# Optimization experiments

Measured on AMD Instinct MI355X. Metric: run time of the kernel, lower is better.

The kernel has to match this reference:

```python
import jax, jax.numpy as jnp
import numpy as np

N_EMBD = 1024
EXPAND = 2
D_INNER = N_EMBD * EXPAND          # 2048
D_STATE = 64
N_HEADS = D_INNER // D_STATE       # 32
HEAD_DIM = D_INNER // N_HEADS      # 64
N_GROUPS = 1
D_CONV = 4
N_LAYERS = 48
BATCH, SEQ = 1, 512
PROJ_SIZE = 2 * D_INNER + N_HEADS + 2 * N_GROUPS * D_STATE  # 4256
EPS = 1e-6


def setup_inputs() -> dict:
    key = jax.random.key(0)
    ks = jax.random.split(key, 6)
    init_std = 0.02
    proj_std = 0.02 / np.sqrt(2 * N_LAYERS)
    return {
        "x": jax.random.normal(ks[0], (BATCH, SEQ, N_EMBD), jnp.float32),
        "norm_scale": jnp.ones((N_EMBD,), jnp.float32),
        "w_in": jax.random.normal(ks[1], (N_EMBD, PROJ_SIZE), jnp.float32) * init_std,
        "conv_weight": jax.random.normal(ks[2], (D_CONV, D_INNER), jnp.float32) * 0.02,
        "conv_bias": jnp.zeros((D_INNER,), jnp.float32),
        "A_log": jnp.log(0.5 + jnp.arange(N_HEADS, dtype=jnp.float32) * 0.5 / N_HEADS),
        "dt_bias": jax.random.normal(ks[3], (N_HEADS,), jnp.float32) * 0.1,
        "w_out": jax.random.normal(ks[4], (D_INNER, N_EMBD), jnp.float32) * proj_std,
    }


def _mamba_fwd(x, norm_scale, w_in, conv_weight, conv_bias, A_log, dt_bias, w_out):
    b, T, _ = x.shape
    residual = x
    # RMSNorm
    xn = x * jax.lax.rsqrt(jnp.mean(x * x, axis=-1, keepdims=True) + EPS) * norm_scale
    # in_proj and split
    proj = xn @ w_in  # (b, T, proj_size)
    gate = proj[..., :D_INNER]
    ssm_in = proj[..., D_INNER:2 * D_INNER]
    dt_raw = proj[..., 2 * D_INNER:2 * D_INNER + N_HEADS]
    gs = N_GROUPS * D_STATE
    B = proj[..., 2 * D_INNER + N_HEADS:2 * D_INNER + N_HEADS + gs].reshape(b, T, N_GROUPS, D_STATE)
    C = proj[..., 2 * D_INNER + N_HEADS + gs:].reshape(b, T, N_GROUPS, D_STATE)
    # causal depthwise short conv (cross-correlation, matching lax.conv semantics)
    xp = jnp.pad(ssm_in, ((0, 0), (D_CONV - 1, 0), (0, 0)))
    conv = conv_bias + sum(conv_weight[k] * xp[:, k:k + T, :] for k in range(D_CONV))
    h = jax.nn.silu(conv)  # (b, T, d_inner)
    dt = jax.nn.softplus(dt_raw + dt_bias)  # (b, T, H)
    A = -jnp.exp(A_log)  # (H,)
    A_bar = jnp.exp(A[None, None, :] * dt)  # (b, T, H)
    # heads / groups
    hpg = N_HEADS // N_GROUPS
    xh = h.reshape(b, T, N_HEADS, HEAD_DIM)
    Bh = jnp.repeat(B, hpg, axis=2)  # (b, T, H, N)
    Ch = jnp.repeat(C, hpg, axis=2)  # (b, T, H, N)
    # Bu[b,t,h,p,n] = B[b,t,h,n] * dt[b,t,h] * x[b,t,h,p]
    Bu = Bh[:, :, :, None, :] * (dt[..., None, None] * xh[..., None])  # (b,T,H,P,N)

    def _binary_op(left, right):
        a_l, b_l = left
        a_r, b_r = right
        return (a_l * a_r, a_r * b_l + b_r)

    # A_bar broadcast to (b,T,H,1,1) so the pair broadcasts against Bu
    _, states = jax.lax.associative_scan(_binary_op, (A_bar[..., None, None], Bu), axis=1)
    y = jnp.einsum('bthpn,bthn->bthp', states, Ch).reshape(b, T, D_INNER)
    y = y * jax.nn.silu(gate)
    y = y @ w_out
    return residual + y


def reference(x, norm_scale, w_in, conv_weight, conv_bias, A_log, dt_bias, w_out):
    return _mamba_fwd(x, norm_scale, w_in, conv_weight, conv_bias, A_log, dt_bias, w_out)
```

## Files before the change

### kernel.cpp

```cpp
#include <hip/hip_runtime.h>
#include <hip/hip_bf16.h>

typedef unsigned short u16;
typedef float f32x4v __attribute__((ext_vector_type(4)));
typedef short short8 __attribute__((ext_vector_type(8)));

#define TSEQ 512
#define EMB  1024
#define DI   2048
#define NH   32
#define DS   64
#define PROJ 4256
#define PROJP 4352
#define NCH  16
#define LCH  32
#define KSPLIT2 4

__device__ __forceinline__ u16 f2bf(float f) {
    union { __hip_bfloat16 h; u16 u; } cv;
    cv.h = __float2bfloat16(f);
    return cv.u;
}
__device__ __forceinline__ unsigned pack2(float a, float b) {
    return (unsigned)f2bf(a) | ((unsigned)f2bf(b) << 16);
}
__device__ __forceinline__ float silu(float v) { return v / (1.f + expf(-v)); }

__device__ __forceinline__ void transpose_tile(
        const float* __restrict__ src, u16* __restrict__ dst,
        int K, int N, int n0, int k0, int tid, float tile[64][68]) {
    const int lr = tid >> 4;
    const int lc = tid & 15;
    #pragma unroll
    for (int ps = 0; ps < 4; ++ps) {
        int r = ps * 16 + lr;
        float4 v;
        if (n0 + lc * 4 + 3 < N) {
            v = *(const float4*)&src[(size_t)(k0 + r) * N + n0 + lc * 4];
        } else {
            float t0 = 0.f, t1 = 0.f, t2 = 0.f, t3 = 0.f;
            int nb = n0 + lc * 4;
            if (nb + 0 < N) t0 = src[(size_t)(k0 + r) * N + nb + 0];
            if (nb + 1 < N) t1 = src[(size_t)(k0 + r) * N + nb + 1];
            if (nb + 2 < N) t2 = src[(size_t)(k0 + r) * N + nb + 2];
            if (nb + 3 < N) t3 = src[(size_t)(k0 + r) * N + nb + 3];
            v = make_float4(t0, t1, t2, t3);
        }
        *(float4*)&tile[r][lc * 4] = v;
    }
    __syncthreads();
    const int kk2 = (tid & 31) * 2;
    const int nr  = tid >> 5;
    #pragma unroll
    for (int ps = 0; ps < 8; ++ps) {
        int n = ps * 8 + nr;
        unsigned o = (unsigned)f2bf(tile[kk2][n]) | ((unsigned)f2bf(tile[kk2 + 1][n]) << 16);
        *(unsigned*)&dst[(size_t)(n0 + n) * K + k0 + kk2] = o;
    }
}

__global__ __launch_bounds__(256) void k_prep(
        const float* __restrict__ w_in, u16* __restrict__ w_inT,
        const float* __restrict__ w_out, u16* __restrict__ w_outT,
        const float* __restrict__ x, const float* __restrict__ scale,
        u16* __restrict__ xnb) {
    __shared__ float tile[64][68];
    const int b = blockIdx.x;
    const int tid = threadIdx.x;
    if (b < 1088) {
        int bx = b % 68, by = b / 68;
        transpose_tile(w_in, w_inT, 1024, PROJ, bx * 64, by * 64, tid, tile);
    } else if (b < 1600) {
        int b2 = b - 1088;
        int bx = b2 % 16, by = b2 / 16;
        transpose_tile(w_out, w_outT, 2048, 1024, bx * 64, by * 64, tid, tile);
    } else {
        int t = b - 1600;
        const float4* xr = (const float4*)(x + (size_t)t * EMB);
        float4 v = xr[tid];
        float ss = v.x * v.x + v.y * v.y + v.z * v.z + v.w * v.w;
        #pragma unroll
        for (int off = 32; off; off >>= 1) ss += __shfl_xor(ss, off);
        if ((tid & 63) == 0) tile[0][tid >> 6] = ss;
        __syncthreads();
        float tot = tile[0][0] + tile[0][1] + tile[0][2] + tile[0][3];
        float inv = rsqrtf(tot * (1.f / EMB) + 1e-6f);
        float4 s = ((const float4*)scale)[tid];
        uint2 o;
        o.x = pack2(v.x * inv * s.x, v.y * inv * s.y);
        o.y = pack2(v.z * inv * s.z, v.w * inv * s.w);
        ((uint2*)xnb)[(size_t)t * 256 + tid] = o;
    }
}

template<int BM, int BN>
__global__ __launch_bounds__(256) void k_gemm(
        const u16* __restrict__ A, int lda,
        const u16* __restrict__ BT, int ldb,
        float* __restrict__ C, int ldc, int Kper) {
    constexpr int WM = BM / 2, WN = BN / 2, FM = WM / 16, FN = WN / 16;
    constexpr int NA = BM * 8 / 256, NB = BN * 8 / 256;
    __shared__ __align__(16) u16 Al[BM][72];
    __shared__ __align__(16) u16 Bl[BN][72];
    const int tid = threadIdx.x;
    const int wid = tid >> 6, lane = tid & 63;
    const int wr = wid >> 1, wc = wid & 1;
    const int ar = lane & 15, kg = lane >> 4;
    const int row0 = blockIdx.y * BM, col0 = blockIdx.x * BN;
    const int kbase = blockIdx.z * Kper;
    const int Mtot = gridDim.y * BM;
    float* Cz = C + (size_t)blockIdx.z * Mtot * ldc;

    short8 ra[NA], rb[NB];
    auto load_stage = [&](int k0) {
        #pragma unroll
        for (int j = 0; j < NA; ++j) {
            int idx = tid + j * 256;
            ra[j] = *(const short8*)(A + (size_t)(row0 + (idx >> 3)) * lda + k0 + (idx & 7) * 8);
        }
        #pragma unroll
        for (int j = 0; j < NB; ++j) {
            int idx = tid + j * 256;
            rb[j] = *(const short8*)(BT + (size_t)(col0 + (idx >> 3)) * ldb + k0 + (idx & 7) * 8);
        }
    };
    auto write_stage = [&]() {
        #pragma unroll
        for (int j = 0; j < NA; ++j) {
            int idx = tid + j * 256;
            *(short8*)&Al[idx >> 3][(idx & 7) * 8] = ra[j];
        }
        #pragma unroll
        for (int j = 0; j < NB; ++j) {
            int idx = tid + j * 256;
            *(short8*)&Bl[idx >> 3][(idx & 7) * 8] = rb[j];
        }
    };

    f32x4v acc[FM][FN] = {};
    const int NT = Kper / 64;
    load_stage(kbase);
    for (int kt = 0; kt < NT; ++kt) {
        write_stage();
        __syncthreads();
        if (kt + 1 < NT) load_stage(kbase + (kt + 1) * 64);
        #pragma unroll
        for (int kk = 0; kk < 2; ++kk) {
            short8 af[FM], bf[FN];
            #pragma unroll
            for (int m = 0; m < FM; ++m)
                af[m] = *(const short8*)&Al[wr * WM + m * 16 + ar][kk * 32 + kg * 8];
            #pragma unroll
            for (int n = 0; n < FN; ++n)
                bf[n] = *(const short8*)&Bl[wc * WN + n * 16 + ar][kk * 32 + kg * 8];
            #pragma unroll
            for (int m = 0; m < FM; ++m)
                #pragma unroll
                for (int n = 0; n < FN; ++n)
                    acc[m][n] = __builtin_amdgcn_mfma_f32_16x16x32_bf16(
                        af[m], bf[n], acc[m][n], 0, 0, 0);
        }
        __syncthreads();
    }
    #pragma unroll
    for (int m = 0; m < FM; ++m)
        #pragma unroll
        for (int n = 0; n < FN; ++n)
            #pragma unroll
            for (int j = 0; j < 4; ++j) {
                int row = row0 + wr * WM + m * 16 + kg * 4 + j;
                int col = col0 + wc * WN + n * 16 + ar;
                Cz[(size_t)row * ldc + col] = acc[m][n][j];
            }
}

__global__ __launch_bounds__(256) void k_reduce_out(
        const float* __restrict__ part, const float* __restrict__ x,
        float* __restrict__ out) {
    int i = blockIdx.x * 256 + threadIdx.x;
    float4 v = ((const float4*)x)[i];
    #pragma unroll
    for (int z = 0; z < KSPLIT2; ++z) {
        float4 p = ((const float4*)part)[(size_t)z * (TSEQ * EMB / 4) + i];
        v.x += p.x; v.y += p.y; v.z += p.z; v.w += p.w;
    }
    ((float4*)out)[i] = v;
}

__global__ __launch_bounds__(1024) void k_scan1g(
        const float* __restrict__ proj, const float* __restrict__ cw,
        const float* __restrict__ cb, const float* __restrict__ A_log,
        const float* __restrict__ dt_bias,
        float* __restrict__ Sloc, float* __restrict__ Pcum,
        float* __restrict__ yloc) {
    const int c = blockIdx.x, h = blockIdx.y;
    const int tid = threadIdx.x;
    const int q = tid & 15, p = tid >> 4, n0 = q * 4;
    __shared__ __align__(16) float Blds[LCH][64];
    __shared__ __align__(16) float Clds[LCH][64];
    __shared__ __align__(16) float dtxl[LCH][64];
    __shared__ __align__(16) float xt[LCH + 3][64];
    __shared__ float al[LCH], dl[LCH];
    __shared__ float yl[LCH][64];
    for (int i = tid; i < (LCH + 3) * 64; i += 1024) {
        int r = i >> 6, n = i & 63;
        int tt = c * LCH - 3 + r;
        xt[r][n] = (tt >= 0) ? proj[(size_t)tt * PROJP + DI + h * 64 + n] : 0.f;
    }
    for (int i = tid; i < LCH * 64; i += 1024) {
        int t = i >> 6, n = i & 63;
        Blds[t][n] = proj[(size_t)(c * LCH + t) * PROJP + 2 * DI + NH + n];
        Clds[t][n] = proj[(size_t)(c * LCH + t) * PROJP + 2 * DI + NH + DS + n];
    }
    if (tid < LCH) {
        float z = proj[(size_t)(c * LCH + tid) * PROJP + 2 * DI + h] + dt_bias[h];
        float dt = (z > 20.f) ? z : log1pf(expf(z));
        dl[tid] = dt;
        al[tid] = expf(-expf(A_log[h]) * dt);
    }
    __syncthreads();
    for (int i = tid; i < LCH * 64; i += 1024) {
        int t = i >> 6, pp = i & 63;
        int ch = h * 64 + pp;
        float cv = cb[ch]
                 + cw[0 * DI + ch] * xt[t][pp]     + cw[1 * DI + ch] * xt[t + 1][pp]
                 + cw[2 * DI + ch] * xt[t + 2][pp] + cw[3 * DI + ch] * xt[t + 3][pp];
        dtxl[t][pp] = dl[t] * silu(cv);
    }
    if (tid < LCH) {
        float pr = 1.f;
        #pragma unroll
        for (int k = 0; k < LCH; ++k) if (k <= tid) pr *= al[k];
        Pcum[((size_t)(c * 32 + h)) * LCH + tid] = pr;
    }
    __syncthreads();
    float4 s = make_float4(0.f, 0.f, 0.f, 0.f);
    #pragma unroll 4
    for (int t = 0; t < LCH; ++t) {
        float a = al[t];
        float dtx = dtxl[t][p];
        float4 b = *(const float4*)&Blds[t][n0];
        float4 cc = *(const float4*)&Clds[t][n0];
        s.x = a * s.x + dtx * b.x;
        s.y = a * s.y + dtx * b.y;
        s.z = a * s.z + dtx * b.z;
        s.w = a * s.w + dtx * b.w;
        float yp = s.x * cc.x + s.y * cc.y + s.z * cc.z + s.w * cc.w;
        yp += __shfl_xor(yp, 1);
        yp += __shfl_xor(yp, 2);
        yp += __shfl_xor(yp, 4);
        yp += __shfl_xor(yp, 8);
        if (q == 0) yl[t][p] = yp;
    }
    *(float4*)&Sloc[((size_t)(c * 32 + h) * 64 + p) * 64 + n0] = s;
    __syncthreads();
    for (int i = tid; i < LCH * 64; i += 1024) {
        int t = i >> 6, pp = i & 63;
        yloc[(size_t)(c * LCH + t) * DI + h * 64 + pp] = yl[t][pp];
    }
}

__global__ __launch_bounds__(256) void k_scan2(
        const float* __restrict__ Sloc, const float* __restrict__ Pcum,
        float* __restrict__ Sinit) {
    int gid = blockIdx.x * 256 + threadIdx.x;
    int h = gid >> 12, rem = gid & 4095;
    float s = 0.f;
    #pragma unroll
    for (int cc = 0; cc < NCH; ++cc) {
        size_t o = (size_t)(cc * 32 + h) * 4096 + rem;
        Sinit[o] = s;
        s = Pcum[((size_t)(cc * 32 + h)) * LCH + (LCH - 1)] * s + Sloc[o];
    }
}

__global__ __launch_bounds__(256) void k_corr(
        const float* __restrict__ proj, const float* __restrict__ Sinit,
        const float* __restrict__ Pcum, const float* __restrict__ yloc,
        u16* __restrict__ yg) {
    const int c = blockIdx.x, h = blockIdx.y;
    const int tid = threadIdx.x;
    const int q = tid & 3, p = tid >> 2, n0 = q * 16;
    __shared__ __align__(16) float Clds[LCH][64];
    __shared__ __align__(16) float Sl[64][68];
    __shared__ float Pl[LCH];
    __shared__ float yl[LCH][64];
    for (int i = tid; i < LCH * 64; i += 256) {
        int t = i >> 6, n = i & 63;
        Clds[t][n] = proj[(size_t)(c * LCH + t) * PROJP + 2 * DI + NH + DS + n];
    }
    for (int i = tid; i < 4096; i += 256) {
        Sl[i >> 6][i & 63] = Sinit[(size_t)(c * 32 + h) * 4096 + i];
    }
    if (tid < LCH) Pl[tid] = Pcum[((size_t)(c * 32 + h)) * LCH + tid];
    __syncthreads();
    float st[16];
    #pragma unroll
    for (int i4 = 0; i4 < 4; ++i4) {
        float4 v = *(const float4*)&Sl[p][n0 + i4 * 4];
        st[i4*4+0] = v.x; st[i4*4+1] = v.y; st[i4*4+2] = v.z; st[i4*4+3] = v.w;
    }
    for (int t = 0; t < LCH; ++t) {
        const float4* crow = (const float4*)&Clds[t][n0];
        float acc = 0.f;
        #pragma unroll
        for (int i4 = 0; i4 < 4; ++i4) {
            float4 cc4 = crow[i4];
            acc += st[i4*4+0] * cc4.x + st[i4*4+1] * cc4.y
                 + st[i4*4+2] * cc4.z + st[i4*4+3] * cc4.w;
        }
        acc += __shfl_xor(acc, 1);
        acc += __shfl_xor(acc, 2);
        if (q == 0) yl[t][p] = acc * Pl[t];
    }
    __syncthreads();
    for (int i = tid; i < LCH * 64; i += 256) {
        int t = i >> 6, pp = i & 63;
        float y = yloc[(size_t)(c * LCH + t) * DI + h * 64 + pp] + yl[t][pp];
        float g = proj[(size_t)(c * LCH + t) * PROJP + h * 64 + pp];
        yg[(size_t)(c * LCH + t) * DI + h * 64 + pp] = f2bf(y * silu(g));
    }
}

extern "C" void kernel_launch(void* const* d_in, const int* in_sizes, int n_in,
                              void* d_out, int out_size, void* d_ws, size_t ws_size,
                              hipStream_t stream) {
    (void)in_sizes; (void)n_in; (void)out_size; (void)ws_size;
    const float* x       = (const float*)d_in[0];
    const float* nscale  = (const float*)d_in[1];
    const float* w_in    = (const float*)d_in[2];
    const float* conv_w  = (const float*)d_in[3];
    const float* conv_b  = (const float*)d_in[4];
    const float* A_log   = (const float*)d_in[5];
    const float* dt_bias = (const float*)d_in[6];
    const float* w_out   = (const float*)d_in[7];
    float* out = (float*)d_out;

    char* wsp = (char*)d_ws;
    auto alloc = [&](size_t bytes) {
        char* ptr = wsp;
        wsp += (bytes + 255) & ~(size_t)255;
        return ptr;
    };
    u16*   w_inT  = (u16*)  alloc((size_t)PROJP * 1024 * 2);
    u16*   w_outT = (u16*)  alloc((size_t)1024 * 2048 * 2);
    u16*   xnb    = (u16*)  alloc((size_t)512 * 1024 * 2);
    float* proj   = (float*)alloc((size_t)512 * PROJP * 4);
    float* Pcum   = (float*)alloc((size_t)NCH * 32 * LCH * 4);
    float* Sloc   = (float*)alloc((size_t)NCH * 32 * 4096 * 4);
    float* Sinit  = (float*)alloc((size_t)NCH * 32 * 4096 * 4);
    float* yloc   = (float*)alloc((size_t)512 * 2048 * 4);
    u16*   yg     = (u16*)  alloc((size_t)512 * 2048 * 2);
    float* part2  = (float*)alloc((size_t)KSPLIT2 * 512 * 1024 * 4);

    k_prep<<<2112, 256, 0, stream>>>(w_in, w_inT, w_out, w_outT, x, nscale, xnb);
    k_gemm<32, 128><<<dim3(34, 16, 1), 256, 0, stream>>>(
        xnb, 1024, w_inT, 1024, proj, PROJP, 1024);
    k_scan1g<<<dim3(NCH, 32), 1024, 0, stream>>>(
        proj, conv_w, conv_b, A_log, dt_bias, Sloc, Pcum, yloc);
    k_scan2<<<512, 256, 0, stream>>>(Sloc, Pcum, Sinit);
    k_corr<<<dim3(NCH, 32), 256, 0, stream>>>(proj, Sinit, Pcum, yloc, yg);
    k_gemm<32, 128><<<dim3(8, 16, KSPLIT2), 256, 0, stream>>>(
        yg, 2048, w_outT, 2048, part2, 1024, 2048 / KSPLIT2);
    k_reduce_out<<<512, 256, 0, stream>>>(part2, x, out);
}
```

Measured before the change: 159.7 us.

## Replace sequential chunk scan with SSD-style MFMA chunked matmuls

Rewrites the intra-chunk selective scan as Mamba2 SSD matrix form. It computes C·Bᵀ with bf16 MFMA, applies the causal decay mask from cumulative log-decay, and then multiplies by dt·x to get local outputs and chunk end states. The inter-chunk correction is also done with MFMA, and chunk length doubles to 64 so there are half as many chunks. This removes the serial per-timestep recurrence and shuffle reductions, at the cost of bf16 rounding on B, C, x and states and exp-based decay factors.

```diff
diff --git a/kernel.cpp b/kernel.cpp
--- a/kernel.cpp
+++ b/kernel.cpp
@@ -12,9 +12,11 @@
 #define DS   64
 #define PROJ 4256
 #define PROJP 4352
-#define NCH  16
-#define LCH  32
+#define NCH  8
+#define LCH  64
 #define KSPLIT2 4
+
+#define MFMA16(a, b, c) __builtin_amdgcn_mfma_f32_16x16x32_bf16(a, b, c, 0, 0, 0)
 
 __device__ __forceinline__ u16 f2bf(float f) {
     union { __hip_bfloat16 h; u16 u; } cv;
@@ -157,8 +159,7 @@
             for (int m = 0; m < FM; ++m)
                 #pragma unroll
                 for (int n = 0; n < FN; ++n)
-                    acc[m][n] = __builtin_amdgcn_mfma_f32_16x16x32_bf16(
-                        af[m], bf[n], acc[m][n], 0, 0, 0);
+                    acc[m][n] = MFMA16(af[m], bf[n], acc[m][n]);
         }
         __syncthreads();
     }
@@ -187,81 +188,106 @@
     ((float4*)out)[i] = v;
 }
 
-__global__ __launch_bounds__(1024) void k_scan1g(
+__global__ __launch_bounds__(256) void k_ssd(
         const float* __restrict__ proj, const float* __restrict__ cw,
         const float* __restrict__ cb, const float* __restrict__ A_log,
         const float* __restrict__ dt_bias,
-        float* __restrict__ Sloc, float* __restrict__ Pcum,
+        float* __restrict__ Sloc, float* __restrict__ Lacum,
         float* __restrict__ yloc) {
     const int c = blockIdx.x, h = blockIdx.y;
     const int tid = threadIdx.x;
-    const int q = tid & 15, p = tid >> 4, n0 = q * 4;
-    __shared__ __align__(16) float Blds[LCH][64];
-    __shared__ __align__(16) float Clds[LCH][64];
-    __shared__ __align__(16) float dtxl[LCH][64];
-    __shared__ __align__(16) float xt[LCH + 3][64];
-    __shared__ float al[LCH], dl[LCH];
-    __shared__ float yl[LCH][64];
-    for (int i = tid; i < (LCH + 3) * 64; i += 1024) {
+    const int w = tid >> 6, lane = tid & 63;
+    const int ar = lane & 15, kg = lane >> 4;
+    __shared__ __align__(16) u16 Bl[64][72];
+    __shared__ __align__(16) u16 BlTw[64][72];
+    __shared__ __align__(16) u16 Cl[64][72];
+    __shared__ __align__(16) u16 XlT[64][72];
+    __shared__ __align__(16) u16 Gl[64][72];
+    __shared__ float xt[67][68];
+    __shared__ float la[64], dl[64];
+    for (int i = tid; i < 67 * 64; i += 256) {
         int r = i >> 6, n = i & 63;
-        int tt = c * LCH - 3 + r;
+        int tt = c * 64 - 3 + r;
         xt[r][n] = (tt >= 0) ? proj[(size_t)tt * PROJP + DI + h * 64 + n] : 0.f;
     }
-    for (int i = tid; i < LCH * 64; i += 1024) {
+    if (tid < 64) {
+        float z = proj[(size_t)(c * 64 + tid) * PROJP + 2 * DI + h] + dt_bias[h];
+        dl[tid] = (z > 20.f) ? z : log1pf(expf(z));
+    }
+    __syncthreads();
+    if (tid < 64) {
+        float cum = 0.f;
+        #pragma unroll
+        for (int k = 0; k < 64; ++k) if (k <= tid) cum += dl[k];
+        float lav = -expf(A_log[h]) * cum;
+        la[tid] = lav;
+        Lacum[((size_t)(c * 32 + h)) * 64 + tid] = lav;
+    }
+    __syncthreads();
+    const float la63 = la[63];
+    for (int i = tid; i < 4096; i += 256) {
         int t = i >> 6, n = i & 63;
-        Blds[t][n] = proj[(size_t)(c * LCH + t) * PROJP + 2 * DI + NH + n];
-        Clds[t][n] = proj[(size_t)(c * LCH + t) * PROJP + 2 * DI + NH + DS + n];
-    }
-    if (tid < LCH) {
-        float z = proj[(size_t)(c * LCH + tid) * PROJP + 2 * DI + h] + dt_bias[h];
-        float dt = (z > 20.f) ? z : log1pf(expf(z));
-        dl[tid] = dt;
-        al[tid] = expf(-expf(A_log[h]) * dt);
-    }
-    __syncthreads();
-    for (int i = tid; i < LCH * 64; i += 1024) {
-        int t = i >> 6, pp = i & 63;
-        int ch = h * 64 + pp;
-        float cv = cb[ch]
-                 + cw[0 * DI + ch] * xt[t][pp]     + cw[1 * DI + ch] * xt[t + 1][pp]
-                 + cw[2 * DI + ch] * xt[t + 2][pp] + cw[3 * DI + ch] * xt[t + 3][pp];
-        dtxl[t][pp] = dl[t] * silu(cv);
-    }
-    if (tid < LCH) {
-        float pr = 1.f;
-        #pragma unroll
-        for (int k = 0; k < LCH; ++k) if (k <= tid) pr *= al[k];
-        Pcum[((size_t)(c * 32 + h)) * LCH + tid] = pr;
-    }
-    __syncthreads();
-    float4 s = make_float4(0.f, 0.f, 0.f, 0.f);
-    #pragma unroll 4
-    for (int t = 0; t < LCH; ++t) {
-        float a = al[t];
-        float dtx = dtxl[t][p];
-        float4 b = *(const float4*)&Blds[t][n0];
-        float4 cc = *(const float4*)&Clds[t][n0];
-        s.x = a * s.x + dtx * b.x;
-        s.y = a * s.y + dtx * b.y;
-        s.z = a * s.z + dtx * b.z;
-        s.w = a * s.w + dtx * b.w;
-        float yp = s.x * cc.x + s.y * cc.y + s.z * cc.z + s.w * cc.w;
-        yp += __shfl_xor(yp, 1);
-        yp += __shfl_xor(yp, 2);
-        yp += __shfl_xor(yp, 4);
-        yp += __shfl_xor(yp, 8);
-        if (q == 0) yl[t][p] = yp;
-    }
-    *(float4*)&Sloc[((size_t)(c * 32 + h) * 64 + p) * 64 + n0] = s;
-    __syncthreads();
-    for (int i = tid; i < LCH * 64; i += 1024) {
-        int t = i >> 6, pp = i & 63;
-        yloc[(size_t)(c * LCH + t) * DI + h * 64 + pp] = yl[t][pp];
+        size_t rowoff = (size_t)(c * 64 + t) * PROJP + 2 * DI + NH;
+        float bv = proj[rowoff + n];
+        float cv = proj[rowoff + DS + n];
+        Bl[t][n] = f2bf(bv);
+        Cl[t][n] = f2bf(cv);
+        BlTw[n][t] = f2bf(bv * expf(la63 - la[t]));
+        int ch = h * 64 + n;
+        float conv = cb[ch]
+                   + cw[0 * DI + ch] * xt[t][n]     + cw[1 * DI + ch] * xt[t + 1][n]
+                   + cw[2 * DI + ch] * xt[t + 2][n] + cw[3 * DI + ch] * xt[t + 3][n];
+        XlT[n][t] = f2bf(dl[t] * silu(conv));
+    }
+    __syncthreads();
+    f32x4v accG[4] = {};
+    #pragma unroll
+    for (int kk = 0; kk < 2; ++kk) {
+        short8 af = *(const short8*)&Cl[w * 16 + ar][kk * 32 + kg * 8];
+        #pragma unroll
+        for (int tc = 0; tc < 4; ++tc) {
+            short8 bf = *(const short8*)&Bl[tc * 16 + ar][kk * 32 + kg * 8];
+            accG[tc] = MFMA16(af, bf, accG[tc]);
+        }
+    }
+    #pragma unroll
+    for (int tc = 0; tc < 4; ++tc) {
+        int tp = tc * 16 + ar;
+        #pragma unroll
+        for (int j = 0; j < 4; ++j) {
+            int t = w * 16 + kg * 4 + j;
+            float v = (tp <= t) ? accG[tc][j] * expf(la[t] - la[tp]) : 0.f;
+            Gl[t][tp] = f2bf(v);
+        }
+    }
+    __syncthreads();
+    f32x4v accY[4] = {}, accS[4] = {};
+    #pragma unroll
+    for (int kk = 0; kk < 2; ++kk) {
+        short8 ag = *(const short8*)&Gl[w * 16 + ar][kk * 32 + kg * 8];
+        short8 ab = *(const short8*)&BlTw[w * 16 + ar][kk * 32 + kg * 8];
+        #pragma unroll
+        for (int tc = 0; tc < 4; ++tc) {
+            short8 bx = *(const short8*)&XlT[tc * 16 + ar][kk * 32 + kg * 8];
+            accY[tc] = MFMA16(ag, bx, accY[tc]);
+            accS[tc] = MFMA16(ab, bx, accS[tc]);
+        }
+    }
+    float* slc = Sloc + ((size_t)(c * 32 + h)) * 4096;
+    #pragma unroll
+    for (int tc = 0; tc < 4; ++tc) {
+        int p = tc * 16 + ar;
+        #pragma unroll
+        for (int j = 0; j < 4; ++j) {
+            int r = w * 16 + kg * 4 + j;
+            yloc[(size_t)(c * 64 + r) * DI + h * 64 + p] = accY[tc][j];
+            slc[p * 64 + r] = accS[tc][j];
+        }
     }
 }
 
 __global__ __launch_bounds__(256) void k_scan2(
-        const float* __restrict__ Sloc, const float* __restrict__ Pcum,
+        const float* __restrict__ Sloc, const float* __restrict__ Lacum,
         float* __restrict__ Sinit) {
     int gid = blockIdx.x * 256 + threadIdx.x;
     int h = gid >> 12, rem = gid & 4095;
@@ -270,55 +296,51 @@
     for (int cc = 0; cc < NCH; ++cc) {
         size_t o = (size_t)(cc * 32 + h) * 4096 + rem;
         Sinit[o] = s;
-        s = Pcum[((size_t)(cc * 32 + h)) * LCH + (LCH - 1)] * s + Sloc[o];
-    }
-}
-
-__global__ __launch_bounds__(256) void k_corr(
+        float ptot = expf(Lacum[((size_t)(cc * 32 + h)) * 64 + 63]);
+        s = ptot * s + Sloc[o];
+    }
+}
+
+__global__ __launch_bounds__(256) void k_corr2(
         const float* __restrict__ proj, const float* __restrict__ Sinit,
-        const float* __restrict__ Pcum, const float* __restrict__ yloc,
+        const float* __restrict__ Lacum, const float* __restrict__ yloc,
         u16* __restrict__ yg) {
     const int c = blockIdx.x, h = blockIdx.y;
     const int tid = threadIdx.x;
-    const int q = tid & 3, p = tid >> 2, n0 = q * 16;
-    __shared__ __align__(16) float Clds[LCH][64];
-    __shared__ __align__(16) float Sl[64][68];
-    __shared__ float Pl[LCH];
-    __shared__ float yl[LCH][64];
-    for (int i = tid; i < LCH * 64; i += 256) {
+    const int w = tid >> 6, lane = tid & 63;
+    const int ar = lane & 15, kg = lane >> 4;
+    __shared__ __align__(16) u16 Cl[64][72];
+    __shared__ __align__(16) u16 Sl[64][72];
+    __shared__ float la[64];
+    const float* sic = Sinit + ((size_t)(c * 32 + h)) * 4096;
+    for (int i = tid; i < 4096; i += 256) {
         int t = i >> 6, n = i & 63;
-        Clds[t][n] = proj[(size_t)(c * LCH + t) * PROJP + 2 * DI + NH + DS + n];
-    }
-    for (int i = tid; i < 4096; i += 256) {
-        Sl[i >> 6][i & 63] = Sinit[(size_t)(c * 32 + h) * 4096 + i];
-    }
-    if (tid < LCH) Pl[tid] = Pcum[((size_t)(c * 32 + h)) * LCH + tid];
-    __syncthreads();
-    float st[16];
-    #pragma unroll
-    for (int i4 = 0; i4 < 4; ++i4) {
-        float4 v = *(const float4*)&Sl[p][n0 + i4 * 4];
-        st[i4*4+0] = v.x; st[i4*4+1] = v.y; st[i4*4+2] = v.z; st[i4*4+3] = v.w;
-    }
-    for (int t = 0; t < LCH; ++t) {
-        const float4* crow = (const float4*)&Clds[t][n0];
-        float acc = 0.f;
-        #pragma unroll
-        for (int i4 = 0; i4 < 4; ++i4) {
-            float4 cc4 = crow[i4];
-            acc += st[i4*4+0] * cc4.x + st[i4*4+1] * cc4.y
-                 + st[i4*4+2] * cc4.z + st[i4*4+3] * cc4.w;
-        }
-        acc += __shfl_xor(acc, 1);
-        acc += __shfl_xor(acc, 2);
-        if (q == 0) yl[t][p] = acc * Pl[t];
-    }
-    __syncthreads();
-    for (int i = tid; i < LCH * 64; i += 256) {
-        int t = i >> 6, pp = i & 63;
-        float y = yloc[(size_t)(c * LCH + t) * DI + h * 64 + pp] + yl[t][pp];
-        float g = proj[(size_t)(c * LCH + t) * PROJP + h * 64 + pp];
-        yg[(size_t)(c * LCH + t) * DI + h * 64 + pp] = f2bf(y * silu(g));
+        Cl[t][n] = f2bf(proj[(size_t)(c * 64 + t) * PROJP + 2 * DI + NH + DS + n]);
+        Sl[t][n] = f2bf(sic[i]);
+    }
+    if (tid < 64) la[tid] = Lacum[((size_t)(c * 32 + h)) * 64 + tid];
+    __syncthreads();
+    f32x4v acc[4] = {};
+    #pragma unroll
+    for (int kk = 0; kk < 2; ++kk) {
+        short8 ac = *(const short8*)&Cl[w * 16 + ar][kk * 32 + kg * 8];
+        #pragma unroll
+        for (int tc = 0; tc < 4; ++tc) {
+            short8 bs = *(const short8*)&Sl[tc * 16 + ar][kk * 32 + kg * 8];
+            acc[tc] = MFMA16(ac, bs, acc[tc]);
+        }
+    }
+    #pragma unroll
+    for (int tc = 0; tc < 4; ++tc) {
+        int p = tc * 16 + ar;
+        #pragma unroll
+        for (int j = 0; j < 4; ++j) {
+            int t = w * 16 + kg * 4 + j;
+            float y = yloc[(size_t)(c * 64 + t) * DI + h * 64 + p]
+                    + expf(la[t]) * acc[tc][j];
+            float g = proj[(size_t)(c * 64 + t) * PROJP + h * 64 + p];
+            yg[(size_t)(c * 64 + t) * DI + h * 64 + p] = f2bf(y * silu(g));
+        }
     }
 }
 
@@ -346,7 +368,7 @@
     u16*   w_outT = (u16*)  alloc((size_t)1024 * 2048 * 2);
     u16*   xnb    = (u16*)  alloc((size_t)512 * 1024 * 2);
     float* proj   = (float*)alloc((size_t)512 * PROJP * 4);
-    float* Pcum   = (float*)alloc((size_t)NCH * 32 * LCH * 4);
+    float* Lacum  = (float*)alloc((size_t)NCH * 32 * 64 * 4);
     float* Sloc   = (float*)alloc((size_t)NCH * 32 * 4096 * 4);
     float* Sinit  = (float*)alloc((size_t)NCH * 32 * 4096 * 4);
     float* yloc   = (float*)alloc((size_t)512 * 2048 * 4);
@@ -356,10 +378,10 @@
     k_prep<<<2112, 256, 0, stream>>>(w_in, w_inT, w_out, w_outT, x, nscale, xnb);
     k_gemm<32, 128><<<dim3(34, 16, 1), 256, 0, stream>>>(
         xnb, 1024, w_inT, 1024, proj, PROJP, 1024);
-    k_scan1g<<<dim3(NCH, 32), 1024, 0, stream>>>(
-        proj, conv_w, conv_b, A_log, dt_bias, Sloc, Pcum, yloc);
-    k_scan2<<<512, 256, 0, stream>>>(Sloc, Pcum, Sinit);
-    k_corr<<<dim3(NCH, 32), 256, 0, stream>>>(proj, Sinit, Pcum, yloc, yg);
+    k_ssd<<<dim3(NCH, 32), 256, 0, stream>>>(
+        proj, conv_w, conv_b, A_log, dt_bias, Sloc, Lacum, yloc);
+    k_scan2<<<512, 256, 0, stream>>>(Sloc, Lacum, Sinit);
+    k_corr2<<<dim3(NCH, 32), 256, 0, stream>>>(proj, Sinit, Lacum, yloc, yg);
     k_gemm<32, 128><<<dim3(8, 16, KSPLIT2), 256, 0, stream>>>(
         yg, 2048, w_outT, 2048, part2, 1024, 2048 / KSPLIT2);
     k_reduce_out<<<512, 256, 0, stream>>>(part2, x, out);
```

After: 143.9 us. -9.9%, faster.
